# Performance work log

Hardware: AMD Instinct MI355X
Metric: run time of the kernel (lower is better)

The kernel has to match this reference:

```python
import jax, jax.numpy as jnp
import numpy as np

B, C, H, W = 8, 128, 64, 64


def _conv1x1(t, w, b):
    # t: [B,C,H,W], w: [O,C], b: [O]  (torch Conv2d k=1 weight squeezed)
    return jnp.einsum('bchw,oc->bohw', t, w) + b[None, :, None, None]


def setup_inputs() -> dict:
    key = jax.random.key(0)
    ks = jax.random.split(key, 6)
    s = 1.0 / np.sqrt(C)  # conv init scale
    return {
        'x': jax.random.normal(ks[0], (B, C, H, W), dtype=jnp.float32),
        'freq_weights': jnp.ones((C,), dtype=jnp.float32),
        'wq': jax.random.normal(ks[1], (C, C), dtype=jnp.float32) * s,
        'bq': jnp.zeros((C,), dtype=jnp.float32),
        'wk': jax.random.normal(ks[2], (C, C), dtype=jnp.float32) * s,
        'bk': jnp.zeros((C,), dtype=jnp.float32),
        'wv': jax.random.normal(ks[3], (C, C), dtype=jnp.float32) * s,
        'bv': jnp.zeros((C,), dtype=jnp.float32),
        'wo': jax.random.normal(ks[4], (C, C), dtype=jnp.float32) * s,
        'bo': jnp.zeros((C,), dtype=jnp.float32),
    }


def reference(x, freq_weights, wq, bq, wk, bk, wv, bv, wo, bo):
    b, c, h, w = x.shape
    n = h * w
    # FFT-domain magnitude reweighting (faithful abs/angle reconstruction)
    fd = jnp.fft.fft2(x, axes=(-2, -1))
    mag = jnp.abs(fd)
    freq_attn = mag * freq_weights[None, :, None, None]
    refined_freq = freq_attn * jnp.exp(1j * jnp.angle(fd))
    refined = jnp.fft.ifft2(refined_freq, axes=(-2, -1)).real.astype(x.dtype)
    # 1x1-conv Q/K/V projections
    q = _conv1x1(refined, wq, bq).reshape(b, c, n)
    k = _conv1x1(refined, wk, bk).reshape(b, c, n)
    v = _conv1x1(refined, wv, bv).reshape(b, c, n)
    # Spatial self-attention over HW tokens, features = channels
    scores = jnp.einsum('bcn,bcm->bnm', q, k) / jnp.sqrt(jnp.asarray(c, x.dtype))
    attn = jax.nn.softmax(scores, axis=-1)  # [B, HW, HW]
    out = jnp.einsum('bnm,bcm->bcn', attn, v).reshape(b, c, h, w)
    return _conv1x1(out, wo, bo)
```

## Files before the change

### kernel.cpp

```cpp
#include <hip/hip_runtime.h>
#include <hip/hip_bf16.h>
#include <math.h>


typedef __bf16 bf16;
typedef _Float16 f16;
typedef __bf16 bf16x8 __attribute__((ext_vector_type(8)));
typedef __bf16 bf16x4 __attribute__((ext_vector_type(4)));
typedef __bf16 bf16x2 __attribute__((ext_vector_type(2)));
typedef _Float16 f16x8 __attribute__((ext_vector_type(8)));
typedef float  f32x4  __attribute__((ext_vector_type(4)));
typedef unsigned int u32x4 __attribute__((ext_vector_type(4)));

#define MFMA16(a, b, c) __builtin_amdgcn_mfma_f32_16x16x32_bf16((a), (b), (c), 0, 0, 0)

static constexpr int BATCH = 8;
static constexpr int CH    = 128;
static constexpr int NTOK  = 4096;
static constexpr int XS    = 136;
static constexpr int VS    = 72;
static constexpr int PS    = 72;
static constexpr int MS    = 136;
static constexpr float FIXM = 8.0f;

__device__ inline bf16x8 cvt8(const float* p, float s) {
  f32x4 a = *(const f32x4*)p;
  f32x4 b = *(const f32x4*)(p + 4);
  bf16x8 r;
  #pragma unroll
  for (int i = 0; i < 4; ++i) { r[i] = (bf16)(a[i] * s); r[4 + i] = (bf16)(b[i] * s); }
  return r;
}

__global__ __launch_bounds__(512) void proj_kernel(
    const float* __restrict__ x, const float* __restrict__ fw,
    const float* __restrict__ wq, const float* __restrict__ wk,
    const float* __restrict__ wv,
    const float* __restrict__ bq, const float* __restrict__ bk,
    const float* __restrict__ bv,
    bf16* __restrict__ Qt, bf16* __restrict__ Kt, bf16* __restrict__ Vt,
    float qscale)
{
  const int wg = blockIdx.x;
  const int b = wg >> 6, tile = wg & 63;
  const int t = threadIdx.x;
  const int w = t >> 6, lane = t & 63, quad = lane >> 4, l15 = lane & 15;

  __shared__ bf16 stage[128 * VS];

  const float* xb = x + (size_t)b * CH * NTOK + tile * 64;
  #pragma unroll
  for (int i = 0; i < 8; ++i) {
    int c = (i * 8 + w) * 2;
    float f0 = fw[c], f1 = fw[c + 1];
    float x0 = xb[(size_t)c * NTOK + lane] * f0;
    float x1 = xb[(size_t)(c + 1) * NTOK + lane] * f1;
    bf16x2 pk; pk.x = (bf16)x0; pk.y = (bf16)x1;
    *(bf16x2*)(&stage[lane * XS + c]) = pk;
  }
  __syncthreads();

  bf16x8 xfrag[4][4];
  #pragma unroll
  for (int st = 0; st < 4; ++st)
    #pragma unroll
    for (int ks = 0; ks < 4; ++ks)
      xfrag[st][ks] = *(const bf16x8*)(&stage[(st * 16 + l15) * XS + ks * 32 + quad * 8]);

  const size_t wrow = (size_t)(w * 16 + l15) * CH;
  const int tokb = tile * 64;
  __syncthreads();

  {
    bf16x8 qw[4];
    #pragma unroll
    for (int ks = 0; ks < 4; ++ks) qw[ks] = cvt8(wq + wrow + ks * 32 + quad * 8, qscale);
    f32x4 acc[4];
    #pragma unroll
    for (int st = 0; st < 4; ++st) acc[st] = (f32x4){0.f, 0.f, 0.f, 0.f};
    #pragma unroll
    for (int ks = 0; ks < 4; ++ks)
      #pragma unroll
      for (int st = 0; st < 4; ++st)
        acc[st] = MFMA16(qw[ks], xfrag[st][ks], acc[st]);
    float bias[4];
    #pragma unroll
    for (int r = 0; r < 4; ++r) bias[r] = bq[w * 16 + quad * 4 + r] * qscale;
    #pragma unroll
    for (int st = 0; st < 4; ++st) {
      bf16x4 o;
      #pragma unroll
      for (int r = 0; r < 4; ++r) o[r] = (bf16)(acc[st][r] + bias[r]);
      *(bf16x4*)(&stage[(st * 16 + l15) * XS + w * 16 + quad * 4]) = o;
    }
    __syncthreads();
    #pragma unroll
    for (int p = 0; p < 2; ++p) {
      int idx = p * 512 + t, row = idx >> 4, ch = (idx & 15) * 8;
      u32x4 d = *(const u32x4*)(&stage[row * XS + ch]);
      *(u32x4*)(&Qt[((size_t)b * NTOK + tokb + row) * CH + ch]) = d;
    }
    __syncthreads();
  }
  {
    bf16x8 kw[4];
    #pragma unroll
    for (int ks = 0; ks < 4; ++ks) kw[ks] = cvt8(wk + wrow + ks * 32 + quad * 8, 1.0f);
    f32x4 acc[4];
    #pragma unroll
    for (int st = 0; st < 4; ++st) acc[st] = (f32x4){0.f, 0.f, 0.f, 0.f};
    #pragma unroll
    for (int ks = 0; ks < 4; ++ks)
      #pragma unroll
      for (int st = 0; st < 4; ++st)
        acc[st] = MFMA16(kw[ks], xfrag[st][ks], acc[st]);
    float bias[4];
    #pragma unroll
    for (int r = 0; r < 4; ++r) bias[r] = bk[w * 16 + quad * 4 + r];
    #pragma unroll
    for (int st = 0; st < 4; ++st) {
      bf16x4 o;
      #pragma unroll
      for (int r = 0; r < 4; ++r) o[r] = (bf16)(acc[st][r] + bias[r]);
      *(bf16x4*)(&stage[(st * 16 + l15) * XS + w * 16 + quad * 4]) = o;
    }
    __syncthreads();
    #pragma unroll
    for (int p = 0; p < 2; ++p) {
      int idx = p * 512 + t, row = idx >> 4, ch = (idx & 15) * 8;
      u32x4 d = *(const u32x4*)(&stage[row * XS + ch]);
      *(u32x4*)(&Kt[((size_t)b * NTOK + tokb + row) * CH + ch]) = d;
    }
    __syncthreads();
  }
  {
    bf16x8 vw[4];
    #pragma unroll
    for (int ks = 0; ks < 4; ++ks) vw[ks] = cvt8(wv + wrow + ks * 32 + quad * 8, 1.0f);
    f32x4 acc[4];
    #pragma unroll
    for (int st = 0; st < 4; ++st) acc[st] = (f32x4){0.f, 0.f, 0.f, 0.f};
    #pragma unroll
    for (int ks = 0; ks < 4; ++ks)
      #pragma unroll
      for (int st = 0; st < 4; ++st)
        acc[st] = MFMA16(xfrag[st][ks], vw[ks], acc[st]);
    float bias = bv[w * 16 + l15];
    #pragma unroll
    for (int st = 0; st < 4; ++st) {
      bf16x4 o;
      #pragma unroll
      for (int r = 0; r < 4; ++r) o[r] = (bf16)(acc[st][r] + bias);
      *(bf16x4*)(&stage[(w * 16 + l15) * VS + st * 16 + quad * 4]) = o;
    }
    __syncthreads();
    #pragma unroll
    for (int p = 0; p < 2; ++p) {
      int idx = p * 512 + t, row = idx >> 3, tk = (idx & 7) * 8;
      u32x4 d = *(const u32x4*)(&stage[row * VS + tk]);
      *(u32x4*)(&Vt[((size_t)b * CH + row) * NTOK + tokb + tk]) = d;
    }
  }
}

__global__ __launch_bounds__(256, 2) void flash_part_kernel(
    const bf16* __restrict__ Qt, const bf16* __restrict__ Kt,
    const bf16* __restrict__ Vt, f16* __restrict__ Op, float* __restrict__ Lp)
{
  const int wg = blockIdx.x;
  const int b = wg >> 6, half = (wg >> 5) & 1, qt = wg & 31;
  const int t = threadIdx.x;
  const int w = t >> 6, lane = t & 63, quad = lane >> 4, l15 = lane & 15;
  const int swz = l15 & 7;

  __shared__ bf16 ldsK[64 * 128];
  __shared__ bf16 ldsV[128 * 64];
  __shared__ bf16 ldsP[4 * 32 * PS];

  bf16x8 qfrag[2][4];
  #pragma unroll
  for (int s2 = 0; s2 < 2; ++s2) {
    const bf16* qb = Qt + ((size_t)b * NTOK + qt * 128 + w * 32 + s2 * 16 + l15) * CH;
    #pragma unroll
    for (int ks = 0; ks < 4; ++ks)
      qfrag[s2][ks] = *(const bf16x8*)(qb + ks * 32 + quad * 8);
  }

  f32x4 o_acc[2][8];
  #pragma unroll
  for (int s2 = 0; s2 < 2; ++s2)
    #pragma unroll
    for (int nt = 0; nt < 8; ++nt) o_acc[s2][nt] = (f32x4){0.f, 0.f, 0.f, 0.f};
  float lsum[2] = {0.f, 0.f};

  const bf16* kb = Kt + ((size_t)b * NTOK + half * 2048) * CH;
  const bf16* vb = Vt + (size_t)b * CH * NTOK + half * 2048;
  bf16* Pw = ldsP + w * 32 * PS;

  const bf16* kg[4]; bf16* kl[4];
  const bf16* vg[4]; bf16* vl[4];
  #pragma unroll
  for (int i = 0; i < 4; ++i) {
    int idx = t + i * 256;
    { int row = idx >> 4, cb = idx & 15;
      kg[i] = kb + (size_t)idx * 8;
      kl[i] = &ldsK[row * 128 + ((cb ^ (row & 7)) * 8)]; }
    { int row = idx >> 3, cb = idx & 7;
      vg[i] = vb + (size_t)row * NTOK + cb * 8;
      vl[i] = &ldsV[row * 64 + ((cb ^ (row & 7)) * 8)]; }
  }

  u32x4 rk[4], rv[4];
  #pragma unroll
  for (int i = 0; i < 4; ++i) {
    rk[i] = *(const u32x4*)kg[i];
    rv[i] = *(const u32x4*)vg[i];
    kg[i] += 64 * CH;
    vg[i] += 64;
  }

  for (int kt = 0; kt < 32; ++kt) {
    __syncthreads();
    #pragma unroll
    for (int i = 0; i < 4; ++i) {
      *(u32x4*)kl[i] = rk[i];
      *(u32x4*)vl[i] = rv[i];
    }
    __syncthreads();

    if (kt < 31) {
      #pragma unroll
      for (int i = 0; i < 4; ++i) {
        rk[i] = *(const u32x4*)kg[i];
        rv[i] = *(const u32x4*)vg[i];
        kg[i] += 64 * CH;
        vg[i] += 64;
      }
    }

    #pragma unroll
    for (int mt = 0; mt < 4; ++mt) {
      f32x4 s[2];
      s[0] = (f32x4){0.f, 0.f, 0.f, 0.f};
      s[1] = (f32x4){0.f, 0.f, 0.f, 0.f};
      #pragma unroll
      for (int ks = 0; ks < 4; ++ks) {
        bf16x8 kfr = *(const bf16x8*)(&ldsK[(mt * 16 + l15) * 128 + (((ks * 4 + quad) ^ swz) * 8)]);
        s[0] = MFMA16(kfr, qfrag[0][ks], s[0]);
        s[1] = MFMA16(kfr, qfrag[1][ks], s[1]);
      }
      #pragma unroll
      for (int s2 = 0; s2 < 2; ++s2) {
        f32x4 v = s[s2];
        bf16x4 pk;
        float ps = 0.f;
        #pragma unroll
        for (int r = 0; r < 4; ++r) {
          float p = exp2f(v[r] - FIXM);
          ps += p;
          pk[r] = (bf16)p;
        }
        lsum[s2] += ps;
        *(bf16x4*)(&Pw[(s2 * 16 + l15) * PS + mt * 16 + quad * 4]) = pk;
      }
    }

    bf16x8 pfrag[2][2];
    #pragma unroll
    for (int s2 = 0; s2 < 2; ++s2)
      #pragma unroll
      for (int c = 0; c < 2; ++c)
        pfrag[s2][c] = *(const bf16x8*)(&Pw[(s2 * 16 + l15) * PS + c * 32 + quad * 8]);

    #pragma unroll
    for (int k2 = 0; k2 < 2; ++k2)
      #pragma unroll
      for (int nt = 0; nt < 8; ++nt) {
        bf16x8 vfr = *(const bf16x8*)(&ldsV[(nt * 16 + l15) * 64 + (((k2 * 4 + quad) ^ swz) * 8)]);
        o_acc[0][nt] = MFMA16(pfrag[0][k2], vfr, o_acc[0][nt]);
        o_acc[1][nt] = MFMA16(pfrag[1][k2], vfr, o_acc[1][nt]);
      }
  }

  const size_t obase = ((size_t)(b * 2 + half) * NTOK + qt * 128 + w * 32) * CH;
  #pragma unroll
  for (int s2 = 0; s2 < 2; ++s2)
    #pragma unroll
    for (int nt = 0; nt < 8; ++nt)
      #pragma unroll
      for (int r = 0; r < 4; ++r) {
        int row = s2 * 16 + quad * 4 + r;
        Op[obase + (size_t)row * CH + nt * 16 + l15] = (f16)o_acc[s2][nt][r];
      }
  #pragma unroll
  for (int s2 = 0; s2 < 2; ++s2) {
    float v = lsum[s2];
    v += __shfl_xor(v, 16);
    v += __shfl_xor(v, 32);
    if (quad == 0)
      Lp[(size_t)(b * 2 + half) * NTOK + qt * 128 + w * 32 + s2 * 16 + l15] = v;
  }
}

__global__ __launch_bounds__(256) void merge_kernel(
    const f16* __restrict__ Op, const float* __restrict__ Lp,
    const float* __restrict__ wo, const float* __restrict__ bo,
    float* __restrict__ out)
{
  const int wg = blockIdx.x;
  const int b = wg >> 6, tile = wg & 63;
  const int t = threadIdx.x;
  const int w = t >> 6, lane = t & 63, quad = lane >> 4, l15 = lane & 15;

  __shared__ bf16 ldsO[64 * MS];

  const f16* o0 = Op + ((size_t)(b * 2 + 0) * NTOK + tile * 64) * CH;
  const f16* o1 = Op + ((size_t)(b * 2 + 1) * NTOK + tile * 64) * CH;
  const float* lp0 = Lp + (size_t)(b * 2 + 0) * NTOK + tile * 64;
  const float* lp1 = Lp + (size_t)(b * 2 + 1) * NTOK + tile * 64;

  #pragma unroll
  for (int i = 0; i < 4; ++i) {
    int idx = t + i * 256;
    int row = idx >> 4, cb = idx & 15;
    float inv = 1.0f / (lp0[row] + lp1[row]);
    f16x8 a0 = *(const f16x8*)(o0 + (size_t)row * CH + cb * 8);
    f16x8 a1 = *(const f16x8*)(o1 + (size_t)row * CH + cb * 8);
    bf16 tmp[8];
    #pragma unroll
    for (int j = 0; j < 8; ++j)
      tmp[j] = (bf16)(((float)a0[j] + (float)a1[j]) * inv);
    *(u32x4*)(&ldsO[row * MS + cb * 8]) = *(u32x4*)tmp;
  }
  __syncthreads();

  #pragma unroll
  for (int mi = 0; mi < 2; ++mi) {
    int mt = w * 2 + mi;
    f32x4 facc[4];
    #pragma unroll
    for (int nt = 0; nt < 4; ++nt) facc[nt] = (f32x4){0.f, 0.f, 0.f, 0.f};
    #pragma unroll
    for (int ks = 0; ks < 4; ++ks) {
      bf16x8 afr = cvt8(wo + (size_t)(mt * 16 + l15) * CH + ks * 32 + quad * 8, 1.0f);
      #pragma unroll
      for (int nt = 0; nt < 4; ++nt) {
        bf16x8 bfr = *(const bf16x8*)(&ldsO[(nt * 16 + l15) * MS + ks * 32 + quad * 8]);
        facc[nt] = MFMA16(afr, bfr, facc[nt]);
      }
    }
    #pragma unroll
    for (int nt = 0; nt < 4; ++nt) {
      int n = tile * 64 + nt * 16 + l15;
      #pragma unroll
      for (int r = 0; r < 4; ++r) {
        int o = mt * 16 + quad * 4 + r;
        out[((size_t)b * CH + o) * NTOK + n] = facc[nt][r] + bo[o];
      }
    }
  }
}

extern "C" void kernel_launch(void* const* d_in, const int* in_sizes, int n_in,
                              void* d_out, int out_size, void* d_ws, size_t ws_size,
                              hipStream_t stream)
{
  const float* x  = (const float*)d_in[0];
  const float* fw = (const float*)d_in[1];
  const float* wq = (const float*)d_in[2];
  const float* bq = (const float*)d_in[3];
  const float* wk = (const float*)d_in[4];
  const float* bk = (const float*)d_in[5];
  const float* wv = (const float*)d_in[6];
  const float* bv = (const float*)d_in[7];
  const float* wo = (const float*)d_in[8];
  const float* bo = (const float*)d_in[9];
  float* out = (float*)d_out;

  char* ws = (char*)d_ws;
  bf16*  Qt  = (bf16*)ws;
  bf16*  Kt  = Qt + (size_t)BATCH * NTOK * CH;
  bf16*  Vt  = Kt + (size_t)BATCH * NTOK * CH;
  f16*   Op  = (f16*)(ws + 3ull * 8388608);
  float* Lp  = (float*)((char*)Op + 16777216);

  const float qscale = 0.08838834764831845f * 1.44269504f;

  proj_kernel<<<512, 512, 0, stream>>>(x, fw, wq, wk, wv,
                                       bq, bk, bv, Qt, Kt, Vt, qscale);
  flash_part_kernel<<<512, 256, 0, stream>>>(Qt, Kt, Vt, Op, Lp);
  merge_kernel<<<512, 256, 0, stream>>>(Op, Lp, wo, bo, out);
}
```

Before: 192.0 us.

## Fuse split-KV merge and output projection into flash kernel via atomic tickets

Removes the separate merge kernel. Each flash workgroup takes an atomic ticket per (batch, query tile), and the second of the two split-KV halves to finish performs the merge and the output 1x1 projection for its 128 tokens. The aim is to cut one kernel launch and the tail/gap between kernels. The cost is a memset launch, a threadfence plus atomic per workgroup, and serialized merge work on half the workgroups, which could lengthen the tail.

Result: slower. 282.1 us (+46.9%).

```diff
diff --git a/kernel.cpp b/kernel.cpp
--- a/kernel.cpp
+++ b/kernel.cpp
@@ -163,19 +163,23 @@
   }
 }
 
-__global__ __launch_bounds__(256, 2) void flash_part_kernel(
+__global__ __launch_bounds__(256, 2) void flash_merge_kernel(
     const bf16* __restrict__ Qt, const bf16* __restrict__ Kt,
-    const bf16* __restrict__ Vt, f16* __restrict__ Op, float* __restrict__ Lp)
+    const bf16* __restrict__ Vt, f16* __restrict__ Op, float* __restrict__ Lp,
+    const float* __restrict__ wo, const float* __restrict__ bo,
+    float* __restrict__ out, unsigned int* __restrict__ ticket)
 {
+  __shared__ __align__(16) char ldsbuf[51264];
+  bf16* ldsK = (bf16*)ldsbuf;
+  bf16* ldsV = (bf16*)(ldsbuf + 16384);
+  bf16* ldsP = (bf16*)(ldsbuf + 32768);
+  unsigned int* s_flag = (unsigned int*)(ldsbuf + 51200);
+
   const int wg = blockIdx.x;
   const int b = wg >> 6, half = (wg >> 5) & 1, qt = wg & 31;
   const int t = threadIdx.x;
   const int w = t >> 6, lane = t & 63, quad = lane >> 4, l15 = lane & 15;
   const int swz = l15 & 7;
-
-  __shared__ bf16 ldsK[64 * 128];
-  __shared__ bf16 ldsV[128 * 64];
-  __shared__ bf16 ldsP[4 * 32 * PS];
 
   bf16x8 qfrag[2][4];
   #pragma unroll
@@ -300,64 +304,63 @@
     if (quad == 0)
       Lp[(size_t)(b * 2 + half) * NTOK + qt * 128 + w * 32 + s2 * 16 + l15] = v;
   }
-}
-
-__global__ __launch_bounds__(256) void merge_kernel(
-    const f16* __restrict__ Op, const float* __restrict__ Lp,
-    const float* __restrict__ wo, const float* __restrict__ bo,
-    float* __restrict__ out)
-{
-  const int wg = blockIdx.x;
-  const int b = wg >> 6, tile = wg & 63;
-  const int t = threadIdx.x;
-  const int w = t >> 6, lane = t & 63, quad = lane >> 4, l15 = lane & 15;
-
-  __shared__ bf16 ldsO[64 * MS];
-
-  const f16* o0 = Op + ((size_t)(b * 2 + 0) * NTOK + tile * 64) * CH;
-  const f16* o1 = Op + ((size_t)(b * 2 + 1) * NTOK + tile * 64) * CH;
-  const float* lp0 = Lp + (size_t)(b * 2 + 0) * NTOK + tile * 64;
-  const float* lp1 = Lp + (size_t)(b * 2 + 1) * NTOK + tile * 64;
-
-  #pragma unroll
-  for (int i = 0; i < 4; ++i) {
-    int idx = t + i * 256;
-    int row = idx >> 4, cb = idx & 15;
-    float inv = 1.0f / (lp0[row] + lp1[row]);
-    f16x8 a0 = *(const f16x8*)(o0 + (size_t)row * CH + cb * 8);
-    f16x8 a1 = *(const f16x8*)(o1 + (size_t)row * CH + cb * 8);
-    bf16 tmp[8];
-    #pragma unroll
-    for (int j = 0; j < 8; ++j)
-      tmp[j] = (bf16)(((float)a0[j] + (float)a1[j]) * inv);
-    *(u32x4*)(&ldsO[row * MS + cb * 8]) = *(u32x4*)tmp;
-  }
+
+  __threadfence();
+  if (t == 0) *s_flag = atomicAdd(&ticket[b * 32 + qt], 1u);
   __syncthreads();
-
-  #pragma unroll
-  for (int mi = 0; mi < 2; ++mi) {
-    int mt = w * 2 + mi;
-    f32x4 facc[4];
-    #pragma unroll
-    for (int nt = 0; nt < 4; ++nt) facc[nt] = (f32x4){0.f, 0.f, 0.f, 0.f};
-    #pragma unroll
-    for (int ks = 0; ks < 4; ++ks) {
-      bf16x8 afr = cvt8(wo + (size_t)(mt * 16 + l15) * CH + ks * 32 + quad * 8, 1.0f);
+  if (*s_flag != 1u) return;
+  __threadfence();
+
+  bf16* ldsO = (bf16*)ldsbuf;
+  #pragma unroll
+  for (int j = 0; j < 2; ++j) {
+    const int tile = qt * 2 + j;
+    const f16* o0 = Op + ((size_t)(b * 2 + 0) * NTOK + tile * 64) * CH;
+    const f16* o1 = Op + ((size_t)(b * 2 + 1) * NTOK + tile * 64) * CH;
+    const float* lp0 = Lp + (size_t)(b * 2 + 0) * NTOK + tile * 64;
+    const float* lp1 = Lp + (size_t)(b * 2 + 1) * NTOK + tile * 64;
+
+    #pragma unroll
+    for (int i = 0; i < 4; ++i) {
+      int idx = t + i * 256;
+      int row = idx >> 4, cb = idx & 15;
+      float inv = 1.0f / (lp0[row] + lp1[row]);
+      f16x8 a0 = *(const f16x8*)(o0 + (size_t)row * CH + cb * 8);
+      f16x8 a1 = *(const f16x8*)(o1 + (size_t)row * CH + cb * 8);
+      bf16 tmp[8];
+      #pragma unroll
+      for (int jj = 0; jj < 8; ++jj)
+        tmp[jj] = (bf16)(((float)a0[jj] + (float)a1[jj]) * inv);
+      *(u32x4*)(&ldsO[row * MS + cb * 8]) = *(u32x4*)tmp;
+    }
+    __syncthreads();
+
+    #pragma unroll
+    for (int mi = 0; mi < 2; ++mi) {
+      int mt = w * 2 + mi;
+      f32x4 facc[4];
+      #pragma unroll
+      for (int nt = 0; nt < 4; ++nt) facc[nt] = (f32x4){0.f, 0.f, 0.f, 0.f};
+      #pragma unroll
+      for (int ks = 0; ks < 4; ++ks) {
+        bf16x8 afr = cvt8(wo + (size_t)(mt * 16 + l15) * CH + ks * 32 + quad * 8, 1.0f);
+        #pragma unroll
+        for (int nt = 0; nt < 4; ++nt) {
+          bf16x8 bfr = *(const bf16x8*)(&ldsO[(nt * 16 + l15) * MS + ks * 32 + quad * 8]);
+          facc[nt] = MFMA16(afr, bfr, facc[nt]);
+        }
+      }
       #pragma unroll
       for (int nt = 0; nt < 4; ++nt) {
-        bf16x8 bfr = *(const bf16x8*)(&ldsO[(nt * 16 + l15) * MS + ks * 32 + quad * 8]);
-        facc[nt] = MFMA16(afr, bfr, facc[nt]);
-      }
-    }
-    #pragma unroll
-    for (int nt = 0; nt < 4; ++nt) {
-      int n = tile * 64 + nt * 16 + l15;
-      #pragma unroll
-      for (int r = 0; r < 4; ++r) {
-        int o = mt * 16 + quad * 4 + r;
-        out[((size_t)b * CH + o) * NTOK + n] = facc[nt][r] + bo[o];
-      }
-    }
+        int n = tile * 64 + nt * 16 + l15;
+        #pragma unroll
+        for (int r = 0; r < 4; ++r) {
+          int o = mt * 16 + quad * 4 + r;
+          out[((size_t)b * CH + o) * NTOK + n] = facc[nt][r] + bo[o];
+        }
+      }
+    }
+    __syncthreads();
   }
 }
 
@@ -383,11 +386,14 @@
   bf16*  Vt  = Kt + (size_t)BATCH * NTOK * CH;
   f16*   Op  = (f16*)(ws + 3ull * 8388608);
   float* Lp  = (float*)((char*)Op + 16777216);
+  unsigned int* ticket = (unsigned int*)((char*)Lp + 262144);
+
+  hipMemsetAsync(ticket, 0, 256 * sizeof(unsigned int), stream);
 
   const float qscale = 0.08838834764831845f * 1.44269504f;
 
   proj_kernel<<<512, 512, 0, stream>>>(x, fw, wq, wk, wv,
                                        bq, bk, bv, Qt, Kt, Vt, qscale);
-  flash_part_kernel<<<512, 256, 0, stream>>>(Qt, Kt, Vt, Op, Lp);
-  merge_kernel<<<512, 256, 0, stream>>>(Op, Lp, wo, bo, out);
+  flash_merge_kernel<<<512, 256, 0, stream>>>(Qt, Kt, Vt, Op, Lp,
+                                              wo, bo, out, ticket);
 }
```

## Enlarge flash query tiles, split keys into slabs, double-buffer K/V via direct LDS DMA

Applied to the files above, without the earlier changes.

Each workgroup now handles 256 queries (64 per wave) with 32-key tiles, and the key range is split into up to 4 slabs chosen by workspace size, with merge_kernel summing a variable number of partials. K/V tiles are loaded with global_load_lds straight into double-buffered LDS with rotated/XOR swizzles, replacing register staging and removing one barrier per iteration. The aim is more MFMA work per K/V fragment load and better overlap of loads with compute. The cost is higher register pressure (four o_acc row groups), more partial-output traffic when S=4, and reliance on the DMA write layout matching the swizzled reads.

Result: no change. 193.5 us (+0.8%).

```diff
diff --git a/kernel.cpp b/kernel.cpp
--- a/kernel.cpp
+++ b/kernel.cpp
@@ -19,9 +19,15 @@
 static constexpr int NTOK  = 4096;
 static constexpr int XS    = 136;
 static constexpr int VS    = 72;
-static constexpr int PS    = 72;
+static constexpr int PS2   = 40;
 static constexpr int MS    = 136;
 static constexpr float FIXM = 8.0f;
+
+__device__ inline void dma16(const bf16* g, bf16* l) {
+  __builtin_amdgcn_global_load_lds(
+      (__attribute__((address_space(1))) unsigned int*)g,
+      (__attribute__((address_space(3))) unsigned int*)l, 16, 0, 0);
+}
 
 __device__ inline bf16x8 cvt8(const float* p, float s) {
   f32x4 a = *(const f32x4*)p;
@@ -165,147 +171,141 @@
 
 __global__ __launch_bounds__(256, 2) void flash_part_kernel(
     const bf16* __restrict__ Qt, const bf16* __restrict__ Kt,
-    const bf16* __restrict__ Vt, f16* __restrict__ Op, float* __restrict__ Lp)
+    const bf16* __restrict__ Vt, f16* __restrict__ Op, float* __restrict__ Lp,
+    int nslab, int ntile)
 {
+  __shared__ __align__(16) char lds[53248];
+
   const int wg = blockIdx.x;
-  const int b = wg >> 6, half = (wg >> 5) & 1, qt = wg & 31;
+  const int qt = wg & 15;
+  const int slab = (wg >> 4) % nslab;
+  const int b = wg / (nslab * 16);
   const int t = threadIdx.x;
   const int w = t >> 6, lane = t & 63, quad = lane >> 4, l15 = lane & 15;
   const int swz = l15 & 7;
 
-  __shared__ bf16 ldsK[64 * 128];
-  __shared__ bf16 ldsV[128 * 64];
-  __shared__ bf16 ldsP[4 * 32 * PS];
-
-  bf16x8 qfrag[2][4];
-  #pragma unroll
-  for (int s2 = 0; s2 < 2; ++s2) {
-    const bf16* qb = Qt + ((size_t)b * NTOK + qt * 128 + w * 32 + s2 * 16 + l15) * CH;
+  bf16x8 qfrag[4][4];
+  #pragma unroll
+  for (int s4 = 0; s4 < 4; ++s4) {
+    const bf16* qb = Qt + ((size_t)b * NTOK + qt * 256 + w * 64 + s4 * 16 + l15) * CH;
     #pragma unroll
     for (int ks = 0; ks < 4; ++ks)
-      qfrag[s2][ks] = *(const bf16x8*)(qb + ks * 32 + quad * 8);
-  }
-
-  f32x4 o_acc[2][8];
-  #pragma unroll
-  for (int s2 = 0; s2 < 2; ++s2)
-    #pragma unroll
-    for (int nt = 0; nt < 8; ++nt) o_acc[s2][nt] = (f32x4){0.f, 0.f, 0.f, 0.f};
-  float lsum[2] = {0.f, 0.f};
-
-  const bf16* kb = Kt + ((size_t)b * NTOK + half * 2048) * CH;
-  const bf16* vb = Vt + (size_t)b * CH * NTOK + half * 2048;
-  bf16* Pw = ldsP + w * 32 * PS;
-
-  const bf16* kg[4]; bf16* kl[4];
-  const bf16* vg[4]; bf16* vl[4];
-  #pragma unroll
-  for (int i = 0; i < 4; ++i) {
-    int idx = t + i * 256;
-    { int row = idx >> 4, cb = idx & 15;
-      kg[i] = kb + (size_t)idx * 8;
-      kl[i] = &ldsK[row * 128 + ((cb ^ (row & 7)) * 8)]; }
-    { int row = idx >> 3, cb = idx & 7;
-      vg[i] = vb + (size_t)row * NTOK + cb * 8;
-      vl[i] = &ldsV[row * 64 + ((cb ^ (row & 7)) * 8)]; }
-  }
-
-  u32x4 rk[4], rv[4];
-  #pragma unroll
-  for (int i = 0; i < 4; ++i) {
-    rk[i] = *(const u32x4*)kg[i];
-    rv[i] = *(const u32x4*)vg[i];
-    kg[i] += 64 * CH;
-    vg[i] += 64;
-  }
-
-  for (int kt = 0; kt < 32; ++kt) {
-    __syncthreads();
-    #pragma unroll
-    for (int i = 0; i < 4; ++i) {
-      *(u32x4*)kl[i] = rk[i];
-      *(u32x4*)vl[i] = rv[i];
-    }
-    __syncthreads();
-
-    if (kt < 31) {
-      #pragma unroll
-      for (int i = 0; i < 4; ++i) {
-        rk[i] = *(const u32x4*)kg[i];
-        rv[i] = *(const u32x4*)vg[i];
-        kg[i] += 64 * CH;
-        vg[i] += 64;
+      qfrag[s4][ks] = *(const bf16x8*)(qb + ks * 32 + quad * 8);
+  }
+
+  f32x4 o_acc[4][8];
+  #pragma unroll
+  for (int s4 = 0; s4 < 4; ++s4)
+    #pragma unroll
+    for (int nt = 0; nt < 8; ++nt) o_acc[s4][nt] = (f32x4){0.f, 0.f, 0.f, 0.f};
+  float lsum[4] = {0.f, 0.f, 0.f, 0.f};
+
+  const int koff = slab * ntile * 32;
+  const bf16* kb = Kt + ((size_t)b * NTOK + koff) * CH;
+  const bf16* vb = Vt + (size_t)b * CH * NTOK + koff;
+
+  const bf16* kdma[2]; const bf16* vdma[2];
+  #pragma unroll
+  for (int jj = 0; jj < 2; ++jj) {
+    int slot = w * 128 + jj * 64 + lane;
+    int krow = slot >> 4, kcb = slot & 15;
+    kdma[jj] = kb + (size_t)krow * CH + ((kcb ^ (krow & 7)) * 8);
+    int vch = slot >> 2, vcb = slot & 3;
+    vdma[jj] = vb + (size_t)vch * NTOK + (((vcb + ((vch >> 2) & 3)) & 3) * 8);
+  }
+
+  bf16* Pw = (bf16*)(lds + 32768) + w * 64 * PS2;
+
+  {
+    bf16* dK = (bf16*)(lds) + w * 1024;
+    bf16* dV = (bf16*)(lds + 8192) + w * 1024;
+    dma16(kdma[0], dK); dma16(kdma[1], dK + 512);
+    dma16(vdma[0], dV); dma16(vdma[1], dV + 512);
+    kdma[0] += 32 * CH; kdma[1] += 32 * CH;
+    vdma[0] += 32;      vdma[1] += 32;
+  }
+  __syncthreads();
+
+  for (int kt = 0; kt < ntile; ++kt) {
+    const char* bK = lds + ((kt & 1) ? 16384 : 0);
+    const char* bV = bK + 8192;
+
+    if (kt + 1 < ntile) {
+      bf16* nK = (bf16*)(lds + ((kt & 1) ? 0 : 16384)) + w * 1024;
+      bf16* nV = nK + 4096;
+      dma16(kdma[0], nK); dma16(kdma[1], nK + 512);
+      dma16(vdma[0], nV); dma16(vdma[1], nV + 512);
+      kdma[0] += 32 * CH; kdma[1] += 32 * CH;
+      vdma[0] += 32;      vdma[1] += 32;
+    }
+
+    #pragma unroll
+    for (int mt = 0; mt < 2; ++mt) {
+      f32x4 s[4];
+      #pragma unroll
+      for (int s4 = 0; s4 < 4; ++s4) s[s4] = (f32x4){0.f, 0.f, 0.f, 0.f};
+      #pragma unroll
+      for (int ks = 0; ks < 4; ++ks) {
+        bf16x8 kfr = *(const bf16x8*)(bK + (mt * 16 + l15) * 256 + (((ks * 4 + quad) ^ swz) * 16));
+        #pragma unroll
+        for (int s4 = 0; s4 < 4; ++s4)
+          s[s4] = MFMA16(kfr, qfrag[s4][ks], s[s4]);
       }
-    }
-
-    #pragma unroll
-    for (int mt = 0; mt < 4; ++mt) {
-      f32x4 s[2];
-      s[0] = (f32x4){0.f, 0.f, 0.f, 0.f};
-      s[1] = (f32x4){0.f, 0.f, 0.f, 0.f};
-      #pragma unroll
-      for (int ks = 0; ks < 4; ++ks) {
-        bf16x8 kfr = *(const bf16x8*)(&ldsK[(mt * 16 + l15) * 128 + (((ks * 4 + quad) ^ swz) * 8)]);
-        s[0] = MFMA16(kfr, qfrag[0][ks], s[0]);
-        s[1] = MFMA16(kfr, qfrag[1][ks], s[1]);
-      }
-      #pragma unroll
-      for (int s2 = 0; s2 < 2; ++s2) {
-        f32x4 v = s[s2];
-        bf16x4 pk;
-        float ps = 0.f;
+      #pragma unroll
+      for (int s4 = 0; s4 < 4; ++s4) {
+        f32x4 v = s[s4];
+        bf16x4 pk; float ps = 0.f;
         #pragma unroll
         for (int r = 0; r < 4; ++r) {
           float p = exp2f(v[r] - FIXM);
-          ps += p;
-          pk[r] = (bf16)p;
+          ps += p; pk[r] = (bf16)p;
         }
-        lsum[s2] += ps;
-        *(bf16x4*)(&Pw[(s2 * 16 + l15) * PS + mt * 16 + quad * 4]) = pk;
+        lsum[s4] += ps;
+        *(bf16x4*)(Pw + (s4 * 16 + l15) * PS2 + mt * 16 + quad * 4) = pk;
       }
     }
 
-    bf16x8 pfrag[2][2];
-    #pragma unroll
-    for (int s2 = 0; s2 < 2; ++s2)
-      #pragma unroll
-      for (int c = 0; c < 2; ++c)
-        pfrag[s2][c] = *(const bf16x8*)(&Pw[(s2 * 16 + l15) * PS + c * 32 + quad * 8]);
-
-    #pragma unroll
-    for (int k2 = 0; k2 < 2; ++k2)
-      #pragma unroll
-      for (int nt = 0; nt < 8; ++nt) {
-        bf16x8 vfr = *(const bf16x8*)(&ldsV[(nt * 16 + l15) * 64 + (((k2 * 4 + quad) ^ swz) * 8)]);
-        o_acc[0][nt] = MFMA16(pfrag[0][k2], vfr, o_acc[0][nt]);
-        o_acc[1][nt] = MFMA16(pfrag[1][k2], vfr, o_acc[1][nt]);
+    bf16x8 pfrag[4];
+    #pragma unroll
+    for (int s4 = 0; s4 < 4; ++s4)
+      pfrag[s4] = *(const bf16x8*)(Pw + (s4 * 16 + l15) * PS2 + quad * 8);
+    const int vrot = (l15 >> 2) & 3;
+    const char* vrb = bV + l15 * 64 + (((quad - vrot) & 3) * 16);
+    #pragma unroll
+    for (int nt = 0; nt < 8; ++nt) {
+      bf16x8 vfr = *(const bf16x8*)(vrb + nt * 1024);
+      #pragma unroll
+      for (int s4 = 0; s4 < 4; ++s4)
+        o_acc[s4][nt] = MFMA16(pfrag[s4], vfr, o_acc[s4][nt]);
+    }
+
+    __syncthreads();
+  }
+
+  const size_t obase = ((size_t)(slab * BATCH + b) * NTOK + qt * 256 + w * 64) * CH;
+  #pragma unroll
+  for (int s4 = 0; s4 < 4; ++s4)
+    #pragma unroll
+    for (int nt = 0; nt < 8; ++nt)
+      #pragma unroll
+      for (int r = 0; r < 4; ++r) {
+        int row = s4 * 16 + quad * 4 + r;
+        Op[obase + (size_t)row * CH + nt * 16 + l15] = (f16)o_acc[s4][nt][r];
       }
-  }
-
-  const size_t obase = ((size_t)(b * 2 + half) * NTOK + qt * 128 + w * 32) * CH;
-  #pragma unroll
-  for (int s2 = 0; s2 < 2; ++s2)
-    #pragma unroll
-    for (int nt = 0; nt < 8; ++nt)
-      #pragma unroll
-      for (int r = 0; r < 4; ++r) {
-        int row = s2 * 16 + quad * 4 + r;
-        Op[obase + (size_t)row * CH + nt * 16 + l15] = (f16)o_acc[s2][nt][r];
-      }
-  #pragma unroll
-  for (int s2 = 0; s2 < 2; ++s2) {
-    float v = lsum[s2];
+  #pragma unroll
+  for (int s4 = 0; s4 < 4; ++s4) {
+    float v = lsum[s4];
     v += __shfl_xor(v, 16);
     v += __shfl_xor(v, 32);
     if (quad == 0)
-      Lp[(size_t)(b * 2 + half) * NTOK + qt * 128 + w * 32 + s2 * 16 + l15] = v;
+      Lp[(size_t)(slab * BATCH + b) * NTOK + qt * 256 + w * 64 + s4 * 16 + l15] = v;
   }
 }
 
 __global__ __launch_bounds__(256) void merge_kernel(
     const f16* __restrict__ Op, const float* __restrict__ Lp,
     const float* __restrict__ wo, const float* __restrict__ bo,
-    float* __restrict__ out)
+    float* __restrict__ out, int nslab)
 {
   const int wg = blockIdx.x;
   const int b = wg >> 6, tile = wg & 63;
@@ -314,22 +314,27 @@
 
   __shared__ bf16 ldsO[64 * MS];
 
-  const f16* o0 = Op + ((size_t)(b * 2 + 0) * NTOK + tile * 64) * CH;
-  const f16* o1 = Op + ((size_t)(b * 2 + 1) * NTOK + tile * 64) * CH;
-  const float* lp0 = Lp + (size_t)(b * 2 + 0) * NTOK + tile * 64;
-  const float* lp1 = Lp + (size_t)(b * 2 + 1) * NTOK + tile * 64;
+  const size_t slabO = (size_t)BATCH * NTOK * CH;
+  const size_t slabL = (size_t)BATCH * NTOK;
+  const f16* ob = Op + ((size_t)b * NTOK + tile * 64) * CH;
+  const float* lp = Lp + (size_t)b * NTOK + tile * 64;
 
   #pragma unroll
   for (int i = 0; i < 4; ++i) {
     int idx = t + i * 256;
     int row = idx >> 4, cb = idx & 15;
-    float inv = 1.0f / (lp0[row] + lp1[row]);
-    f16x8 a0 = *(const f16x8*)(o0 + (size_t)row * CH + cb * 8);
-    f16x8 a1 = *(const f16x8*)(o1 + (size_t)row * CH + cb * 8);
+    float lsum_ = 0.f;
+    for (int s = 0; s < nslab; ++s) lsum_ += lp[s * slabL + row];
+    float acc8[8] = {0.f, 0.f, 0.f, 0.f, 0.f, 0.f, 0.f, 0.f};
+    for (int s = 0; s < nslab; ++s) {
+      f16x8 a = *(const f16x8*)(ob + s * slabO + (size_t)row * CH + cb * 8);
+      #pragma unroll
+      for (int j = 0; j < 8; ++j) acc8[j] += (float)a[j];
+    }
+    float inv = 1.0f / lsum_;
     bf16 tmp[8];
     #pragma unroll
-    for (int j = 0; j < 8; ++j)
-      tmp[j] = (bf16)(((float)a0[j] + (float)a1[j]) * inv);
+    for (int j = 0; j < 8; ++j) tmp[j] = (bf16)(acc8[j] * inv);
     *(u32x4*)(&ldsO[row * MS + cb * 8]) = *(u32x4*)tmp;
   }
   __syncthreads();
@@ -382,12 +387,19 @@
   bf16*  Kt  = Qt + (size_t)BATCH * NTOK * CH;
   bf16*  Vt  = Kt + (size_t)BATCH * NTOK * CH;
   f16*   Op  = (f16*)(ws + 3ull * 8388608);
-  float* Lp  = (float*)((char*)Op + 16777216);
+
+  const size_t qkv_bytes = 3ull * 8388608;
+  const size_t need4 = qkv_bytes + 4ull * ((size_t)BATCH * NTOK * CH * 2 + (size_t)BATCH * NTOK * 4);
+  const int S = (ws_size >= need4) ? 4 : 2;
+  const int ntile = (NTOK / S) / 32;
+
+  float* Lp = (float*)((char*)Op + (size_t)S * BATCH * NTOK * CH * 2);
 
   const float qscale = 0.08838834764831845f * 1.44269504f;
 
   proj_kernel<<<512, 512, 0, stream>>>(x, fw, wq, wk, wv,
                                        bq, bk, bv, Qt, Kt, Vt, qscale);
-  flash_part_kernel<<<512, 256, 0, stream>>>(Qt, Kt, Vt, Op, Lp);
-  merge_kernel<<<512, 256, 0, stream>>>(Op, Lp, wo, bo, out);
-}
+  flash_part_kernel<<<BATCH * S * 16, 256, 0, stream>>>(Qt, Kt, Vt, Op, Lp,
+                                                        S, ntile);
+  merge_kernel<<<512, 256, 0, stream>>>(Op, Lp, wo, bo, out, S);
+}
```

## Double-buffer K/V tiles via direct global-to-LDS DMA in flash attention

Applied to the files above, without the earlier changes.

Replaces the register-staged K/V loads in the flash attention kernel with global_load_lds direct-to-LDS transfers into a double-buffered LDS region. The key tile shrinks from 64 to 32 tokens per iteration, so there are now 64 iterations, each with one barrier instead of two. The swizzle is applied on the global address side so the LDS layout stays conflict-free. The aim is to overlap the next tile's loads with compute and drop the VGPR staging and the extra LDS write pass. In exchange there are more loop iterations with smaller MFMA batches per barrier.

Result: slower. 197.7 us (+3.0%).

```diff
diff --git a/kernel.cpp b/kernel.cpp
--- a/kernel.cpp
+++ b/kernel.cpp
@@ -19,9 +19,15 @@
 static constexpr int NTOK  = 4096;
 static constexpr int XS    = 136;
 static constexpr int VS    = 72;
-static constexpr int PS    = 72;
+static constexpr int PS2   = 40;
 static constexpr int MS    = 136;
 static constexpr float FIXM = 8.0f;
+
+__device__ inline void dma16(const bf16* g, bf16* l) {
+  __builtin_amdgcn_global_load_lds(
+      (__attribute__((address_space(1))) unsigned int*)g,
+      (__attribute__((address_space(3))) unsigned int*)l, 16, 0, 0);
+}
 
 __device__ inline bf16x8 cvt8(const float* p, float s) {
   f32x4 a = *(const f32x4*)p;
@@ -167,16 +173,14 @@
     const bf16* __restrict__ Qt, const bf16* __restrict__ Kt,
     const bf16* __restrict__ Vt, f16* __restrict__ Op, float* __restrict__ Lp)
 {
+  __shared__ __align__(16) char lds[43008];
+
   const int wg = blockIdx.x;
   const int b = wg >> 6, half = (wg >> 5) & 1, qt = wg & 31;
   const int t = threadIdx.x;
   const int w = t >> 6, lane = t & 63, quad = lane >> 4, l15 = lane & 15;
   const int swz = l15 & 7;
 
-  __shared__ bf16 ldsK[64 * 128];
-  __shared__ bf16 ldsV[128 * 64];
-  __shared__ bf16 ldsP[4 * 32 * PS];
-
   bf16x8 qfrag[2][4];
   #pragma unroll
   for (int s2 = 0; s2 < 2; ++s2) {
@@ -195,57 +199,50 @@
 
   const bf16* kb = Kt + ((size_t)b * NTOK + half * 2048) * CH;
   const bf16* vb = Vt + (size_t)b * CH * NTOK + half * 2048;
-  bf16* Pw = ldsP + w * 32 * PS;
-
-  const bf16* kg[4]; bf16* kl[4];
-  const bf16* vg[4]; bf16* vl[4];
-  #pragma unroll
-  for (int i = 0; i < 4; ++i) {
-    int idx = t + i * 256;
-    { int row = idx >> 4, cb = idx & 15;
-      kg[i] = kb + (size_t)idx * 8;
-      kl[i] = &ldsK[row * 128 + ((cb ^ (row & 7)) * 8)]; }
-    { int row = idx >> 3, cb = idx & 7;
-      vg[i] = vb + (size_t)row * NTOK + cb * 8;
-      vl[i] = &ldsV[row * 64 + ((cb ^ (row & 7)) * 8)]; }
-  }
-
-  u32x4 rk[4], rv[4];
-  #pragma unroll
-  for (int i = 0; i < 4; ++i) {
-    rk[i] = *(const u32x4*)kg[i];
-    rv[i] = *(const u32x4*)vg[i];
-    kg[i] += 64 * CH;
-    vg[i] += 64;
-  }
-
-  for (int kt = 0; kt < 32; ++kt) {
-    __syncthreads();
-    #pragma unroll
-    for (int i = 0; i < 4; ++i) {
-      *(u32x4*)kl[i] = rk[i];
-      *(u32x4*)vl[i] = rv[i];
-    }
-    __syncthreads();
-
-    if (kt < 31) {
-      #pragma unroll
-      for (int i = 0; i < 4; ++i) {
-        rk[i] = *(const u32x4*)kg[i];
-        rv[i] = *(const u32x4*)vg[i];
-        kg[i] += 64 * CH;
-        vg[i] += 64;
-      }
-    }
-
-    #pragma unroll
-    for (int mt = 0; mt < 4; ++mt) {
+
+  const bf16* kdma[2]; const bf16* vdma[2];
+  #pragma unroll
+  for (int jj = 0; jj < 2; ++jj) {
+    int slot = w * 128 + jj * 64 + lane;
+    int krow = slot >> 4, kcb = slot & 15;
+    kdma[jj] = kb + (size_t)krow * CH + ((kcb ^ (krow & 7)) * 8);
+    int vch = slot >> 2, vcb = slot & 3;
+    vdma[jj] = vb + (size_t)vch * NTOK + (((vcb + ((vch >> 2) & 3)) & 3) * 8);
+  }
+
+  bf16* Pw = (bf16*)(lds + 32768) + w * 32 * PS2;
+
+  {
+    bf16* dK = (bf16*)(lds) + w * 1024;
+    bf16* dV = (bf16*)(lds + 8192) + w * 1024;
+    dma16(kdma[0], dK); dma16(kdma[1], dK + 512);
+    dma16(vdma[0], dV); dma16(vdma[1], dV + 512);
+    kdma[0] += 32 * CH; kdma[1] += 32 * CH;
+    vdma[0] += 32;      vdma[1] += 32;
+  }
+  __syncthreads();
+
+  for (int kt = 0; kt < 64; ++kt) {
+    const char* bK = lds + ((kt & 1) ? 16384 : 0);
+    const char* bV = bK + 8192;
+
+    if (kt + 1 < 64) {
+      bf16* nK = (bf16*)(lds + ((kt & 1) ? 0 : 16384)) + w * 1024;
+      bf16* nV = nK + 4096;
+      dma16(kdma[0], nK); dma16(kdma[1], nK + 512);
+      dma16(vdma[0], nV); dma16(vdma[1], nV + 512);
+      kdma[0] += 32 * CH; kdma[1] += 32 * CH;
+      vdma[0] += 32;      vdma[1] += 32;
+    }
+
+    #pragma unroll
+    for (int mt = 0; mt < 2; ++mt) {
       f32x4 s[2];
       s[0] = (f32x4){0.f, 0.f, 0.f, 0.f};
       s[1] = (f32x4){0.f, 0.f, 0.f, 0.f};
       #pragma unroll
       for (int ks = 0; ks < 4; ++ks) {
-        bf16x8 kfr = *(const bf16x8*)(&ldsK[(mt * 16 + l15) * 128 + (((ks * 4 + quad) ^ swz) * 8)]);
+        bf16x8 kfr = *(const bf16x8*)(bK + (mt * 16 + l15) * 256 + (((ks * 4 + quad) ^ swz) * 16));
         s[0] = MFMA16(kfr, qfrag[0][ks], s[0]);
         s[1] = MFMA16(kfr, qfrag[1][ks], s[1]);
       }
@@ -261,25 +258,25 @@
           pk[r] = (bf16)p;
         }
         lsum[s2] += ps;
-        *(bf16x4*)(&Pw[(s2 * 16 + l15) * PS + mt * 16 + quad * 4]) = pk;
-      }
-    }
-
-    bf16x8 pfrag[2][2];
+        *(bf16x4*)(Pw + (s2 * 16 + l15) * PS2 + mt * 16 + quad * 4) = pk;
+      }
+    }
+
+    bf16x8 pfrag[2];
     #pragma unroll
     for (int s2 = 0; s2 < 2; ++s2)
-      #pragma unroll
-      for (int c = 0; c < 2; ++c)
-        pfrag[s2][c] = *(const bf16x8*)(&Pw[(s2 * 16 + l15) * PS + c * 32 + quad * 8]);
-
-    #pragma unroll
-    for (int k2 = 0; k2 < 2; ++k2)
-      #pragma unroll
-      for (int nt = 0; nt < 8; ++nt) {
-        bf16x8 vfr = *(const bf16x8*)(&ldsV[(nt * 16 + l15) * 64 + (((k2 * 4 + quad) ^ swz) * 8)]);
-        o_acc[0][nt] = MFMA16(pfrag[0][k2], vfr, o_acc[0][nt]);
-        o_acc[1][nt] = MFMA16(pfrag[1][k2], vfr, o_acc[1][nt]);
-      }
+      pfrag[s2] = *(const bf16x8*)(Pw + (s2 * 16 + l15) * PS2 + quad * 8);
+
+    const int vrot = (l15 >> 2) & 3;
+    const char* vrb = bV + l15 * 64 + (((quad - vrot) & 3) * 16);
+    #pragma unroll
+    for (int nt = 0; nt < 8; ++nt) {
+      bf16x8 vfr = *(const bf16x8*)(vrb + nt * 1024);
+      o_acc[0][nt] = MFMA16(pfrag[0], vfr, o_acc[0][nt]);
+      o_acc[1][nt] = MFMA16(pfrag[1], vfr, o_acc[1][nt]);
+    }
+
+    __syncthreads();
   }
 
   const size_t obase = ((size_t)(b * 2 + half) * NTOK + qt * 128 + w * 32) * CH;
```
